# Optimization experiments

Hardware: AMD Instinct MI355X
Metric: run time of the kernel (lower is better)

Reference implementation:

```python
import jax, jax.numpy as jnp
import numpy as np

NUM_EXPERTS = 8
CAPACITY = 320  # per-batch per-expert token capacity


def setup_inputs() -> dict:
    key = jax.random.key(0)
    k0, k1, k2, k3 = jax.random.split(key, 4)
    B, S, D, F = 4, 2048, 1024, 4096
    E = NUM_EXPERTS
    hidden_states = jax.random.normal(k0, (B, S, D), dtype=jnp.float32)
    gate_w = jax.random.normal(k1, (E, D), dtype=jnp.float32) * 0.02
    w1 = jax.random.normal(k2, (E, D, F), dtype=jnp.float32) * 0.02
    w2 = jax.random.normal(k3, (E, F, D), dtype=jnp.float32) * 0.02
    return {"hidden_states": hidden_states, "gate_w": gate_w, "w1": w1, "w2": w2}


def reference(hidden_states, gate_w, w1, w2):
    E, C = NUM_EXPERTS, CAPACITY
    B, S, D = hidden_states.shape

    # --- route ---
    router_logits = jnp.einsum('bsd,ed->bse', hidden_states, gate_w)
    router_probs = jax.nn.softmax(router_logits, axis=-1)
    expert_idx = jnp.argmax(router_probs, axis=-1)                      # [B,S]
    onehot = jax.nn.one_hot(expert_idx, E, dtype=jnp.int32)             # [B,S,E]
    priority = jnp.cumsum(onehot, axis=1)                               # [B,S,E]
    router_mask = onehot * (priority <= C)                              # [B,S,E]
    assigned = jnp.sum(router_mask, axis=-1) > 0                        # [B,S]
    # slot within expert buffer; dropped tokens go to overflow slot C
    slot = jnp.where(assigned, jnp.sum(priority * onehot, axis=-1) - 1, C)  # [B,S]
    top_prob = jnp.max(router_probs, axis=-1, keepdims=True)            # [B,S,1]

    # --- dispatch: scatter tokens into [B,E,C+1,D] buffers ---
    def dispatch(x_b, e_b, s_b):
        return jnp.zeros((E, C + 1, D), x_b.dtype).at[e_b, s_b].set(x_b)
    buf = jax.vmap(dispatch)(hidden_states, expert_idx, slot)           # [B,E,C+1,D]

    # --- per-expert FFN as grouped GEMM ---
    h = jax.nn.silu(jnp.einsum('becd,edf->becf', buf, w1))
    y = jnp.einsum('becf,efd->becd', h, w2)                             # [B,E,C+1,D]

    # --- combine: gather expert outputs back to token order ---
    gathered = jax.vmap(lambda y_b, e_b, s_b: y_b[e_b, s_b])(y, expert_idx, slot)  # [B,S,D]
    next_states = jnp.where(assigned[..., None], gathered, hidden_states)
    out = top_prob * next_states

    # argmax of capacity-masked one-hot: dropped tokens -> expert 0
    expert_index = jnp.where(assigned, expert_idx, 0)
    return out, router_logits, expert_index
```

## Files before the change

kernel.cpp:

```cpp
#include <hip/hip_runtime.h>

#define B_  4
#define S_  2048
#define D_  1024
#define F_  4096
#define E_  8
#define C_  320
#define CP_ 384
#define NT_ (B_*S_)
#define G_  (B_*E_)

typedef short bf16x8 __attribute__((ext_vector_type(8)));
typedef float f32x4  __attribute__((ext_vector_type(4)));

using gptr_t = const __attribute__((address_space(1))) void*;
using lptr_t = __attribute__((address_space(3))) void*;

__device__ static inline void gll16(const void* g, void* l) {
    __builtin_amdgcn_global_load_lds((gptr_t)g, (lptr_t)l, 16, 0, 0);
}

__device__ static inline unsigned short f2b(float f) {
    unsigned int u = __float_as_uint(f);
    u += 0x7fffu + ((u >> 16) & 1u);
    return (unsigned short)(u >> 16);
}

__global__ __launch_bounds__(256) void k_transpose(const float* __restrict__ in,
                                                   unsigned short* __restrict__ out,
                                                   int R, int Cc) {
    __shared__ unsigned short tile[32][33];
    int e = blockIdx.z;
    const float* src = in + (size_t)e * R * Cc;
    unsigned short* dst = out + (size_t)e * R * Cc;
    int c0 = blockIdx.x * 32, r0 = blockIdx.y * 32;
    int tx = threadIdx.x & 31, ty = threadIdx.x >> 5;
#pragma unroll
    for (int i = 0; i < 32; i += 8)
        tile[ty + i][tx] = f2b(src[(size_t)(r0 + ty + i) * Cc + c0 + tx]);
    __syncthreads();
#pragma unroll
    for (int i = 0; i < 32; i += 8)
        dst[(size_t)(c0 + ty + i) * R + r0 + tx] = tile[tx][ty + i];
}

__global__ __launch_bounds__(256) void k_router(const float* __restrict__ hs,
                                                const float* __restrict__ gw,
                                                float* __restrict__ logits,
                                                int* __restrict__ eidx,
                                                float* __restrict__ tp) {
    int tok  = (int)((blockIdx.x * 256 + threadIdx.x) >> 6);
    int lane = threadIdx.x & 63;
    const float* x = hs + (size_t)tok * D_;
    double acc[E_];
#pragma unroll
    for (int e = 0; e < E_; e++) acc[e] = 0.0;
    for (int i = 0; i < 16; i++) {
        float xv = x[lane + 64 * i];
#pragma unroll
        for (int e = 0; e < E_; e++)
            acc[e] += (double)xv * (double)gw[e * D_ + lane + 64 * i];
    }
#pragma unroll
    for (int e = 0; e < E_; e++) {
#pragma unroll
        for (int off = 32; off > 0; off >>= 1)
            acc[e] += __shfl_xor(acc[e], off, 64);
    }
    if (lane == 0) {
        float l[E_];
        float mx = -1e30f; int am = 0;
#pragma unroll
        for (int e = 0; e < E_; e++) {
            l[e] = (float)acc[e];
            if (l[e] > mx) { mx = l[e]; am = e; }
        }
        float se = 0.f;
#pragma unroll
        for (int e = 0; e < E_; e++) se += __expf(l[e] - mx);
        tp[tok]   = 1.0f / se;
        eidx[tok] = am;
#pragma unroll
        for (int e = 0; e < E_; e++) logits[(size_t)tok * E_ + e] = l[e];
    }
}

__global__ __launch_bounds__(256) void k_scan(const int* __restrict__ eidx,
                                              int* __restrict__ slot,
                                              int* __restrict__ tok_list,
                                              int* __restrict__ counts,
                                              float* __restrict__ eif) {
    int b = blockIdx.x;
    __shared__ int cCnt[32][E_];
    __shared__ int cBase[32][E_];
    int t = threadIdx.x, wv = t >> 6, lane = t & 63;
    const int* eb = eidx + b * S_;
    for (int c = wv; c < 32; c += 4) {
        int e = eb[c * 64 + lane];
#pragma unroll
        for (int x = 0; x < E_; x++) {
            unsigned long long m = __ballot(e == x);
            if (lane == 0) cCnt[c][x] = __popcll(m);
        }
    }
    __syncthreads();
    if (t < E_) {
        int s = 0;
        for (int c = 0; c < 32; c++) { cBase[c][t] = s; s += cCnt[c][t]; }
        counts[b * E_ + t] = s;
    }
    __syncthreads();
    for (int c = wv; c < 32; c += 4) {
        int s_tok = c * 64 + lane;
        int e = eb[s_tok];
        unsigned long long lowmask = (1ull << lane) - 1ull;
        int rank = 0;
#pragma unroll
        for (int x = 0; x < E_; x++) {
            unsigned long long m = __ballot(e == x);
            if (x == e) rank = __popcll(m & lowmask);
        }
        int pos = cBase[c][e] + rank;
        int assigned = (pos < C_);
        slot[b * S_ + s_tok] = assigned ? pos : C_;
        if (assigned) tok_list[(b * E_ + e) * C_ + pos] = s_tok;
        eif[b * S_ + s_tok] = assigned ? (float)e : 0.0f;
    }
}

__global__ __launch_bounds__(256) void k_dispatch(const float* __restrict__ hs,
                                                  const int* __restrict__ tok_list,
                                                  const int* __restrict__ counts,
                                                  unsigned short* __restrict__ Xd) {
    int w    = (int)((blockIdx.x * 256 + threadIdx.x) >> 6);
    int lane = threadIdx.x & 63;
    int g = w / CP_, row = w % CP_;
    int b = g >> 3;
    int n = min(counts[g], C_);
    unsigned short* drow = Xd + ((size_t)g * CP_ + row) * D_;
    if (row < n) {
        int ts = tok_list[g * C_ + row];
        const float* src = hs + ((size_t)b * S_ + ts) * D_;
#pragma unroll
        for (int i = 0; i < 2; i++) {
            int c0 = (lane + 64 * i) * 8;
            float4 v0 = *(const float4*)(src + c0);
            float4 v1 = *(const float4*)(src + c0 + 4);
            uint4 pk;
            pk.x = (unsigned)f2b(v0.x) | ((unsigned)f2b(v0.y) << 16);
            pk.y = (unsigned)f2b(v0.z) | ((unsigned)f2b(v0.w) << 16);
            pk.z = (unsigned)f2b(v1.x) | ((unsigned)f2b(v1.y) << 16);
            pk.w = (unsigned)f2b(v1.z) | ((unsigned)f2b(v1.w) << 16);
            *(uint4*)(drow + c0) = pk;
        }
    } else {
        uint4 z = {0u, 0u, 0u, 0u};
#pragma unroll
        for (int i = 0; i < 2; i++)
            *(uint4*)(drow + (lane + 64 * i) * 8) = z;
    }
}

__global__ __launch_bounds__(256) void k_ffn1(const unsigned short* __restrict__ Xd,
                                              const unsigned short* __restrict__ w1t,
                                              const int* __restrict__ counts,
                                              unsigned short* __restrict__ h) {
    int g = blockIdx.z;
    int n_tok = min(counts[g], C_);
    int m0 = blockIdx.y * 128;
    if (m0 >= n_tok) return;
    int n0 = blockIdx.x * 128;
    int e = g & 7;

    __shared__ unsigned short As[128 * 32];
    __shared__ unsigned short Bs[128 * 32];
    int t = threadIdx.x, lane = t & 63, wv = t >> 6, wm = wv >> 1, wn = wv & 1;

    const unsigned short* Ap = Xd  + (size_t)g * CP_ * D_ + (size_t)(m0 + (t >> 2)) * D_ + (t & 3) * 8;
    const unsigned short* Bp = w1t + (size_t)e * F_ * D_  + (size_t)(n0 + (t >> 2)) * D_ + (t & 3) * 8;

    f32x4 acc[4][4];
    f32x4 z = {0.f, 0.f, 0.f, 0.f};
#pragma unroll
    for (int i = 0; i < 4; i++)
#pragma unroll
        for (int j = 0; j < 4; j++) acc[i][j] = z;

    int ar = (wm * 64 + (lane & 15)) * 32 + (lane >> 4) * 8;
    int br = (wn * 64 + (lane & 15)) * 32 + (lane >> 4) * 8;

    for (int kt = 0; kt < D_; kt += 32) {
        __syncthreads();
        gll16(Ap,            (char*)As + wv * 1024);
        gll16(Ap + 64 * D_,  (char*)As + 4096 + wv * 1024);
        gll16(Bp,            (char*)Bs + wv * 1024);
        gll16(Bp + 64 * D_,  (char*)Bs + 4096 + wv * 1024);
        Ap += 32; Bp += 32;
        __syncthreads();
        bf16x8 a[4], bq[4];
#pragma unroll
        for (int i = 0; i < 4; i++) a[i]  = *(const bf16x8*)&As[ar + i * 512];
#pragma unroll
        for (int j = 0; j < 4; j++) bq[j] = *(const bf16x8*)&Bs[br + j * 512];
#pragma unroll
        for (int i = 0; i < 4; i++)
#pragma unroll
            for (int j = 0; j < 4; j++)
                acc[i][j] = __builtin_amdgcn_mfma_f32_16x16x32_bf16(a[i], bq[j], acc[i][j], 0, 0, 0);
    }

    unsigned short* hb = h + (size_t)g * CP_ * F_;
    int crow = m0 + wm * 64 + (lane >> 4) * 4;
    int ccol = n0 + wn * 64 + (lane & 15);
#pragma unroll
    for (int i = 0; i < 4; i++)
#pragma unroll
        for (int r = 0; r < 4; r++) {
            int row = crow + i * 16 + r;
#pragma unroll
            for (int j = 0; j < 4; j++) {
                float v = acc[i][j][r];
                v = v / (1.0f + __expf(-v));
                hb[(size_t)row * F_ + ccol + j * 16] = f2b(v);
            }
        }
}

__global__ __launch_bounds__(256) void k_ffn2(const unsigned short* __restrict__ h,
                                              const unsigned short* __restrict__ w2t,
                                              const int* __restrict__ counts,
                                              const int* __restrict__ tok_list,
                                              const float* __restrict__ tp,
                                              float* __restrict__ out) {
    int g = blockIdx.z;
    int n_tok = min(counts[g], C_);
    int m0 = blockIdx.y * 128;
    if (m0 >= n_tok) return;
    int n0 = blockIdx.x * 128;
    int b = g >> 3, e = g & 7;

    __shared__ unsigned short As[128 * 32];
    __shared__ unsigned short Bs[128 * 32];
    int t = threadIdx.x, lane = t & 63, wv = t >> 6, wm = wv >> 1, wn = wv & 1;

    const unsigned short* Ap = h   + (size_t)g * CP_ * F_ + (size_t)(m0 + (t >> 2)) * F_ + (t & 3) * 8;
    const unsigned short* Bp = w2t + (size_t)e * D_ * F_  + (size_t)(n0 + (t >> 2)) * F_ + (t & 3) * 8;

    f32x4 acc[4][4];
    f32x4 z = {0.f, 0.f, 0.f, 0.f};
#pragma unroll
    for (int i = 0; i < 4; i++)
#pragma unroll
        for (int j = 0; j < 4; j++) acc[i][j] = z;

    int ar = (wm * 64 + (lane & 15)) * 32 + (lane >> 4) * 8;
    int br = (wn * 64 + (lane & 15)) * 32 + (lane >> 4) * 8;

    for (int kt = 0; kt < F_; kt += 32) {
        __syncthreads();
        gll16(Ap,            (char*)As + wv * 1024);
        gll16(Ap + 64 * F_,  (char*)As + 4096 + wv * 1024);
        gll16(Bp,            (char*)Bs + wv * 1024);
        gll16(Bp + 64 * F_,  (char*)Bs + 4096 + wv * 1024);
        Ap += 32; Bp += 32;
        __syncthreads();
        bf16x8 a[4], bq[4];
#pragma unroll
        for (int i = 0; i < 4; i++) a[i]  = *(const bf16x8*)&As[ar + i * 512];
#pragma unroll
        for (int j = 0; j < 4; j++) bq[j] = *(const bf16x8*)&Bs[br + j * 512];
#pragma unroll
        for (int i = 0; i < 4; i++)
#pragma unroll
            for (int j = 0; j < 4; j++)
                acc[i][j] = __builtin_amdgcn_mfma_f32_16x16x32_bf16(a[i], bq[j], acc[i][j], 0, 0, 0);
    }

    int crow = m0 + wm * 64 + (lane >> 4) * 4;
    int ccol = n0 + wn * 64 + (lane & 15);
#pragma unroll
    for (int i = 0; i < 4; i++)
#pragma unroll
        for (int r = 0; r < 4; r++) {
            int row = crow + i * 16 + r;
            if (row < n_tok) {
                int ts = tok_list[g * C_ + row];
                float sc = tp[b * S_ + ts];
                float* orow = out + ((size_t)b * S_ + ts) * D_ + ccol;
#pragma unroll
                for (int j = 0; j < 4; j++)
                    orow[j * 16] = sc * acc[i][j][r];
            }
        }
}

__global__ __launch_bounds__(256) void k_pass(const float* __restrict__ hs,
                                              const int* __restrict__ slot,
                                              const float* __restrict__ tp,
                                              float* __restrict__ out) {
    int tok  = (int)((blockIdx.x * 256 + threadIdx.x) >> 6);
    int lane = threadIdx.x & 63;
    if (slot[tok] < C_) return;
    float sc = tp[tok];
    const float* src = hs + (size_t)tok * D_;
    float* dst = out + (size_t)tok * D_;
#pragma unroll
    for (int i = 0; i < 4; i++) {
        float4 v = *(const float4*)(src + (lane + 64 * i) * 4);
        v.x *= sc; v.y *= sc; v.z *= sc; v.w *= sc;
        *(float4*)(dst + (lane + 64 * i) * 4) = v;
    }
}

extern "C" void kernel_launch(void* const* d_in, const int* in_sizes, int n_in,
                              void* d_out, int out_size, void* d_ws, size_t ws_size,
                              hipStream_t stream) {
    const float* hs = (const float*)d_in[0];
    const float* gw = (const float*)d_in[1];
    const float* w1 = (const float*)d_in[2];
    const float* w2 = (const float*)d_in[3];

    float* out    = (float*)d_out;
    float* logits = out + (size_t)NT_ * D_;
    float* eif    = logits + (size_t)NT_ * E_;

    char* ws = (char*)d_ws;
    int*            eidx     = (int*)(ws + 0);
    int*            slot     = (int*)(ws + 65536);
    float*          tp       = (float*)(ws + 131072);
    int*            tok_list = (int*)(ws + 196608);
    int*            counts   = (int*)(ws + 262144);
    unsigned short* Xd       = (unsigned short*)(ws + 327680);
    unsigned short* w1t      = (unsigned short*)(ws + 33554432ull);
    unsigned short* w2t      = (unsigned short*)(ws + 100663296ull);
    unsigned short* hbuf     = (unsigned short*)(ws + 167772160ull);

    dim3 blk(256);
    k_transpose<<<dim3(F_ / 32, D_ / 32, E_), blk, 0, stream>>>(w1, w1t, D_, F_);
    k_transpose<<<dim3(D_ / 32, F_ / 32, E_), blk, 0, stream>>>(w2, w2t, F_, D_);
    k_router<<<dim3(NT_ / 4), blk, 0, stream>>>(hs, gw, logits, eidx, tp);
    k_scan<<<dim3(B_), blk, 0, stream>>>(eidx, slot, tok_list, counts, eif);
    k_dispatch<<<dim3(G_ * CP_ / 4), blk, 0, stream>>>(hs, tok_list, counts, Xd);
    k_ffn1<<<dim3(F_ / 128, CP_ / 128, G_), blk, 0, stream>>>(Xd, w1t, counts, hbuf);
    k_ffn2<<<dim3(D_ / 128, CP_ / 128, G_), blk, 0, stream>>>(hbuf, w2t, counts, tok_list, tp, out);
    k_pass<<<dim3(NT_ / 4), blk, 0, stream>>>(hs, slot, tp, out);
}
```

Baseline: 614.1 us.

## Widen weight transpose to 64x64 tiles with vector loads, reorder expert groups

The fp32-to-bf16 weight transpose now uses 64x64 tiles, float4 global reads, and 16-byte packed writes in place of 32x32 tiles with scalar accesses. This targets the memory-bound conversion of both weight tensors, which runs on every call. Separately, the FFN kernels remap blockIdx.z so consecutive z indices cover the same expert across the four batches. The intent is to improve L2 reuse of each expert's weights, at the cost of possible LDS bank conflicts in the padded tile layout.

```diff
diff --git a/kernel.cpp b/kernel.cpp
--- a/kernel.cpp
+++ b/kernel.cpp
@@ -26,22 +26,39 @@
     return (unsigned short)(u >> 16);
 }
 
-__global__ __launch_bounds__(256) void k_transpose(const float* __restrict__ in,
-                                                   unsigned short* __restrict__ out,
-                                                   int R, int Cc) {
-    __shared__ unsigned short tile[32][33];
+__global__ __launch_bounds__(256) void k_convT(const float* __restrict__ in,
+                                               unsigned short* __restrict__ out,
+                                               int R, int Cc) {
+    __shared__ unsigned short ld[64][66];
     int e = blockIdx.z;
     const float* src = in + (size_t)e * R * Cc;
     unsigned short* dst = out + (size_t)e * R * Cc;
-    int c0 = blockIdx.x * 32, r0 = blockIdx.y * 32;
-    int tx = threadIdx.x & 31, ty = threadIdx.x >> 5;
-#pragma unroll
-    for (int i = 0; i < 32; i += 8)
-        tile[ty + i][tx] = f2b(src[(size_t)(r0 + ty + i) * Cc + c0 + tx]);
+    int c0 = blockIdx.x * 64, r0 = blockIdx.y * 64;
+    int t = threadIdx.x;
+
+    int rr = t >> 4;
+    int cg = t & 15;
+#pragma unroll
+    for (int p = 0; p < 4; p++) {
+        int row = p * 16 + rr;
+        float4 v = *(const float4*)(src + (size_t)(r0 + row) * Cc + c0 + cg * 4);
+        ld[cg * 4 + 0][row] = f2b(v.x);
+        ld[cg * 4 + 1][row] = f2b(v.y);
+        ld[cg * 4 + 2][row] = f2b(v.z);
+        ld[cg * 4 + 3][row] = f2b(v.w);
+    }
     __syncthreads();
-#pragma unroll
-    for (int i = 0; i < 32; i += 8)
-        dst[(size_t)(c0 + ty + i) * R + r0 + tx] = tile[tx][ty + i];
+
+    int cc = t >> 3;
+    int rg = t & 7;
+#pragma unroll
+    for (int p = 0; p < 2; p++) {
+        int col = p * 32 + cc;
+        const unsigned* lp = (const unsigned*)&ld[col][rg * 8];
+        uint4 w;
+        w.x = lp[0]; w.y = lp[1]; w.z = lp[2]; w.w = lp[3];
+        *(uint4*)(dst + (size_t)(c0 + col) * R + r0 + rg * 8) = w;
+    }
 }
 
 __global__ __launch_bounds__(256) void k_router(const float* __restrict__ hs,
@@ -165,7 +182,8 @@
                                               const unsigned short* __restrict__ w1t,
                                               const int* __restrict__ counts,
                                               unsigned short* __restrict__ h) {
-    int g = blockIdx.z;
+    int zz = blockIdx.z;
+    int g = (zz & 3) * 8 + (zz >> 2);
     int n_tok = min(counts[g], C_);
     int m0 = blockIdx.y * 128;
     if (m0 >= n_tok) return;
@@ -232,7 +250,8 @@
                                               const int* __restrict__ tok_list,
                                               const float* __restrict__ tp,
                                               float* __restrict__ out) {
-    int g = blockIdx.z;
+    int zz = blockIdx.z;
+    int g = (zz & 3) * 8 + (zz >> 2);
     int n_tok = min(counts[g], C_);
     int m0 = blockIdx.y * 128;
     if (m0 >= n_tok) return;
@@ -336,8 +355,8 @@
     unsigned short* hbuf     = (unsigned short*)(ws + 167772160ull);
 
     dim3 blk(256);
-    k_transpose<<<dim3(F_ / 32, D_ / 32, E_), blk, 0, stream>>>(w1, w1t, D_, F_);
-    k_transpose<<<dim3(D_ / 32, F_ / 32, E_), blk, 0, stream>>>(w2, w2t, F_, D_);
+    k_convT<<<dim3(F_ / 64, D_ / 64, E_), blk, 0, stream>>>(w1, w1t, D_, F_);
+    k_convT<<<dim3(D_ / 64, F_ / 64, E_), blk, 0, stream>>>(w2, w2t, F_, D_);
     k_router<<<dim3(NT_ / 4), blk, 0, stream>>>(hs, gw, logits, eidx, tp);
     k_scan<<<dim3(B_), blk, 0, stream>>>(eidx, slot, tok_list, counts, eif);
     k_dispatch<<<dim3(G_ * CP_ / 4), blk, 0, stream>>>(hs, tok_list, counts, Xd);
```

Result: faster. 598.9 us (-2.5%).
